# Optimization experiments

Hardware: AMD Instinct MI355X
Metric: run time of the kernel (lower is better)

The kernel has to match this reference:

```python
import jax, jax.numpy as jnp
import numpy as np

HEADS = 8
DIM_HEAD = 32
SCALE = DIM_HEAD ** -0.5


def setup_inputs() -> dict:
    key = jax.random.key(0)
    k1, k2, k3 = jax.random.split(key, 3)
    B, L, H, W, C = 2, 5, 100, 176, 256
    inner = HEADS * DIM_HEAD  # 256
    x = jax.random.normal(k1, (B, L, H, W, C), dtype=jnp.float32)
    mask = jnp.ones((B, H, W, 1, L), dtype=jnp.float32)
    W_qkv = jax.random.normal(k2, (C, 3 * inner), dtype=jnp.float32) * (C ** -0.5)
    W_out = jax.random.normal(k3, (inner, C), dtype=jnp.float32) * (inner ** -0.5)
    b_out = jnp.zeros((C,), dtype=jnp.float32)
    return {"x": x, "mask": mask, "W_qkv": W_qkv, "W_out": W_out, "b_out": b_out}


def _cav_attention(x, mask, W_qkv, W_out, b_out):
    B, L, H, W, C = x.shape
    # (B, L, H, W, C) -> (B, H, W, L, C)
    xp = jnp.transpose(x, (0, 2, 3, 1, 4))
    qkv = xp @ W_qkv  # (B,H,W,L,3*inner)
    q, k, v = jnp.split(qkv, 3, axis=-1)

    def to_heads(t):  # (B,H,W,L,m*c) -> (B,m,H,W,L,c)
        t = t.reshape(B, H, W, L, HEADS, DIM_HEAD)
        return jnp.transpose(t, (0, 4, 1, 2, 3, 5))

    q, k, v = to_heads(q), to_heads(k), to_heads(v)
    att = jnp.einsum('bmhwic,bmhwjc->bmhwij', q, k) * SCALE
    # mask: (B,H,W,1,L) -> broadcast over heads as (B,1,H,W,1,L)
    att = jnp.where(mask[:, None] == 0, -jnp.inf, att)
    att = jax.nn.softmax(att, axis=-1)
    out = jnp.einsum('bmhwij,bmhwjc->bmhwic', att, v)
    # (B,m,H,W,L,c) -> (B,H,W,L,m*c)
    out = jnp.transpose(out, (0, 2, 3, 4, 1, 5)).reshape(B, H, W, L, HEADS * DIM_HEAD)
    out = out @ W_out + b_out  # dropout is identity in eval mode
    # (B,H,W,L,C) -> (B,L,H,W,C)
    return jnp.transpose(out, (0, 3, 1, 2, 4))


def reference(x, mask, W_qkv, W_out, b_out):
    return _cav_attention(x, mask, W_qkv, W_out, b_out)
```

## Files before the change

kernel.cpp:

```cpp
#include <hip/hip_runtime.h>
#include <hip/hip_bf16.h>

#define LQ 5
#define HQ 100
#define WQ 176
#define HWQ 17600
#define TPB 16
#define ROWS 80
#define NBLK 2200
#define SCALE_QK 0.17677669529663687f

typedef __attribute__((ext_vector_type(8))) short bf16x8;
typedef __attribute__((ext_vector_type(4))) float f32x4;

__device__ __forceinline__ float bf2f(short s) {
  union { unsigned u; float f; } v;
  v.u = ((unsigned)(unsigned short)s) << 16;
  return v.f;
}
__device__ __forceinline__ unsigned short f2bf(float f) {
  union { float f; unsigned u; } v; v.f = f;
  unsigned r = (v.u + 0x7fffu + ((v.u >> 16) & 1u)) >> 16;
  return (unsigned short)r;
}

__global__ void prep_weights(const float* __restrict__ Wqkv,
                             const float* __restrict__ Wout,
                             unsigned short* __restrict__ WqkvT,
                             unsigned short* __restrict__ WoutT) {
  int idx = blockIdx.x * 256 + threadIdx.x;
  if (idx < 256 * 768) {
    int k = idx / 768, n = idx - k * 768;
    WqkvT[n * 256 + k] = f2bf(Wqkv[idx]);
  }
  if (idx < 256 * 256) {
    int k = idx >> 8, n = idx & 255;
    WoutT[n * 256 + k] = f2bf(Wout[idx]);
  }
}

#define SMEM_BYTES 149120

__global__ __launch_bounds__(256, 1)
void cav_attn_fused(const float* __restrict__ x,
                    const float* __restrict__ mask,
                    const unsigned short* __restrict__ WqkvT,
                    const unsigned short* __restrict__ WoutT,
                    const float* __restrict__ b_out,
                    float* __restrict__ out) {
  extern __shared__ char smem[];
  char* A_base = smem;
  char* O_base = smem + 40960;
  unsigned short* QKV = (unsigned short*)(smem + 81920);
  int*   gofs  = (int*)(smem + 148480);
  float* maskv = (float*)(smem + 148800);

  const int tid  = threadIdx.x;
  const int wave = tid >> 6;
  const int lane = tid & 63;
  const int lr   = lane & 15;
  const int lg   = lane >> 4;
  const int tile0 = blockIdx.x * TPB;

  if (tid < ROWS) {
    int tt = tid / LQ;
    int l  = tid - tt * LQ;
    int gt = tile0 + tt;
    int b  = gt / HWQ;
    int rem = gt - b * HWQ;
    int h  = rem / WQ;
    int w  = rem - h * WQ;
    gofs[tid]  = (((b * LQ + l) * HQ + h) * WQ + w) << 8;
    maskv[tid] = mask[((b * HQ + h) * WQ + w) * LQ + l];
  }
  __syncthreads();

  #pragma unroll
  for (int i = 0; i < 20; ++i) {
    int r  = i * 4 + wave;
    int kq = lane;
    f32x4 v = *(const f32x4*)(x + gofs[r] + kq * 4);
    ushort4 pk;
    pk.x = f2bf(v[0]); pk.y = f2bf(v[1]); pk.z = f2bf(v[2]); pk.w = f2bf(v[3]);
    int byte = r * 512 + kq * 8;
    byte ^= (r & 7) << 4;
    *(ushort4*)(A_base + byte) = pk;
  }
  __syncthreads();

  unsigned short* qbuf = QKV + wave * (ROWS * 104);

  #pragma unroll 1
  for (int hi = 0; hi < 2; ++hi) {
    const int head = wave * 2 + hi;
    f32x4 acc[6][5];
    #pragma unroll
    for (int j = 0; j < 6; ++j)
      #pragma unroll
      for (int mt = 0; mt < 5; ++mt)
        acc[j][mt] = (f32x4){0.f, 0.f, 0.f, 0.f};

    const int hb = head * 32;
    const int nb[6] = { hb, hb + 16, 256 + hb, 256 + hb + 16, 512 + hb, 512 + hb + 16 };

    #pragma unroll
    for (int kt = 0; kt < 8; ++kt) {
      bf16x8 a[5];
      #pragma unroll
      for (int mt = 0; mt < 5; ++mt) {
        int row = mt * 16 + lr;
        int byte = row * 512 + kt * 64 + lg * 16;
        byte ^= (row & 7) << 4;
        a[mt] = *(const bf16x8*)(A_base + byte);
      }
      #pragma unroll
      for (int j = 0; j < 6; ++j) {
        bf16x8 bfr = *(const bf16x8*)(WqkvT + (nb[j] + lr) * 256 + kt * 32 + lg * 8);
        #pragma unroll
        for (int mt = 0; mt < 5; ++mt)
          acc[j][mt] = __builtin_amdgcn_mfma_f32_16x16x32_bf16(a[mt], bfr, acc[j][mt], 0, 0, 0);
      }
    }

    __syncthreads();
    #pragma unroll
    for (int j = 0; j < 6; ++j)
      #pragma unroll
      for (int mt = 0; mt < 5; ++mt)
        #pragma unroll
        for (int rg = 0; rg < 4; ++rg) {
          int row = mt * 16 + lg * 4 + rg;
          qbuf[row * 104 + j * 16 + lr] = f2bf(acc[j][mt][rg]);
        }
    __syncthreads();

    #pragma unroll
    for (int ip = 0; ip < 2; ++ip) {
      const int t_ = (ip == 0) ? (lane >> 2) : lane;
      const int i_ = (ip == 0) ? (lane & 3) : 4;
      if (ip == 0 || lane < 16) {
        const int rq = t_ * 5 + i_;
        float q[32];
        #pragma unroll
        for (int ch = 0; ch < 4; ++ch) {
          bf16x8 qv = *(const bf16x8*)(qbuf + rq * 104 + ch * 8);
          #pragma unroll
          for (int e = 0; e < 8; ++e) q[ch * 8 + e] = bf2f(qv[e]);
        }
        float p[5];
        #pragma unroll
        for (int j = 0; j < 5; ++j) {
          const int rk = t_ * 5 + j;
          float d = 0.f;
          #pragma unroll
          for (int ch = 0; ch < 4; ++ch) {
            bf16x8 kv = *(const bf16x8*)(qbuf + rk * 104 + 32 + ch * 8);
            #pragma unroll
            for (int e = 0; e < 8; ++e) d += q[ch * 8 + e] * bf2f(kv[e]);
          }
          d *= SCALE_QK;
          p[j] = (maskv[rk] == 0.0f) ? -1e30f : d;
        }
        float mx = fmaxf(fmaxf(fmaxf(p[0], p[1]), fmaxf(p[2], p[3])), p[4]);
        float sum = 0.f;
        #pragma unroll
        for (int j = 0; j < 5; ++j) { p[j] = __expf(p[j] - mx); sum += p[j]; }
        const float inv = 1.0f / sum;
        float o[32];
        #pragma unroll
        for (int c = 0; c < 32; ++c) o[c] = 0.f;
        #pragma unroll
        for (int j = 0; j < 5; ++j) {
          const int rv = t_ * 5 + j;
          const float pj = p[j] * inv;
          #pragma unroll
          for (int ch = 0; ch < 4; ++ch) {
            bf16x8 vv = *(const bf16x8*)(qbuf + rv * 104 + 64 + ch * 8);
            #pragma unroll
            for (int e = 0; e < 8; ++e) o[ch * 8 + e] += pj * bf2f(vv[e]);
          }
        }
        #pragma unroll
        for (int ch = 0; ch < 8; ++ch) {
          ushort4 pk;
          pk.x = f2bf(o[ch * 4 + 0]); pk.y = f2bf(o[ch * 4 + 1]);
          pk.z = f2bf(o[ch * 4 + 2]); pk.w = f2bf(o[ch * 4 + 3]);
          int byte = rq * 512 + (head * 32 + ch * 4) * 2;
          byte ^= (rq & 7) << 4;
          *(ushort4*)(O_base + byte) = pk;
        }
      }
    }
  }
  __syncthreads();

  f32x4 acc2[4][5];
  #pragma unroll
  for (int j = 0; j < 4; ++j)
    #pragma unroll
    for (int mt = 0; mt < 5; ++mt)
      acc2[j][mt] = (f32x4){0.f, 0.f, 0.f, 0.f};

  #pragma unroll
  for (int kt = 0; kt < 8; ++kt) {
    bf16x8 a[5];
    #pragma unroll
    for (int mt = 0; mt < 5; ++mt) {
      int row = mt * 16 + lr;
      int byte = row * 512 + kt * 64 + lg * 16;
      byte ^= (row & 7) << 4;
      a[mt] = *(const bf16x8*)(O_base + byte);
    }
    #pragma unroll
    for (int j = 0; j < 4; ++j) {
      bf16x8 bfr = *(const bf16x8*)(WoutT + (wave * 64 + j * 16 + lr) * 256 + kt * 32 + lg * 8);
      #pragma unroll
      for (int mt = 0; mt < 5; ++mt)
        acc2[j][mt] = __builtin_amdgcn_mfma_f32_16x16x32_bf16(a[mt], bfr, acc2[j][mt], 0, 0, 0);
    }
  }

  #pragma unroll
  for (int j = 0; j < 4; ++j) {
    const int col = wave * 64 + j * 16 + lr;
    const float bo = b_out[col];
    #pragma unroll
    for (int mt = 0; mt < 5; ++mt)
      #pragma unroll
      for (int rg = 0; rg < 4; ++rg) {
        int row = mt * 16 + lg * 4 + rg;
        out[gofs[row] + col] = acc2[j][mt][rg] + bo;
      }
  }
}

extern "C" void kernel_launch(void* const* d_in, const int* in_sizes, int n_in,
                              void* d_out, int out_size, void* d_ws, size_t ws_size,
                              hipStream_t stream) {
  (void)in_sizes; (void)n_in; (void)out_size; (void)ws_size;
  const float* x     = (const float*)d_in[0];
  const float* mask  = (const float*)d_in[1];
  const float* Wqkv  = (const float*)d_in[2];
  const float* Wout  = (const float*)d_in[3];
  const float* bout  = (const float*)d_in[4];
  float* out = (float*)d_out;

  unsigned short* WqkvT = (unsigned short*)d_ws;
  unsigned short* WoutT = WqkvT + 768 * 256;

  (void)hipFuncSetAttribute((const void*)cav_attn_fused,
                            hipFuncAttributeMaxDynamicSharedMemorySize, SMEM_BYTES);

  prep_weights<<<768, 256, 0, stream>>>(Wqkv, Wout, WqkvT, WoutT);
  cav_attn_fused<<<NBLK, 256, SMEM_BYTES, stream>>>(x, mask, WqkvT, WoutT, bout, out);
}
```

Measured before the change: 386.5 us.

## Halve tokens per block for two blocks per CU and stage coalesced output stores

Each block now handles 8 tokens (40 rows) instead of 16, and shared memory is cut to about 74 KB so that two blocks fit per CU (launch bounds 2). The per-wave QKV staging no longer uses block-wide barriers, and attention runs in a single pass with one row per lane. The output tile goes through shared memory so global stores become row-contiguous f32x4 writes. In exchange, the MFMA tiles are padded from 40 to 48 rows, which adds wasted matrix work, and the padded rows read stale shared memory.

```diff
diff --git a/kernel.cpp b/kernel.cpp
--- a/kernel.cpp
+++ b/kernel.cpp
@@ -5,10 +5,18 @@
 #define HQ 100
 #define WQ 176
 #define HWQ 17600
-#define TPB 16
-#define ROWS 80
-#define NBLK 2200
+#define TPB 8
+#define ROWS 40
+#define NBLK 4400
 #define SCALE_QK 0.17677669529663687f
+
+#define A_OFF 0
+#define O_OFF 20480
+#define QKV_OFF 40960
+#define QBUF_STRIDE 8320
+#define GOFS_OFF 74240
+#define MASK_OFF 74400
+#define SMEM_BYTES 74560
 
 typedef __attribute__((ext_vector_type(8))) short bf16x8;
 typedef __attribute__((ext_vector_type(4))) float f32x4;
@@ -39,9 +47,7 @@
   }
 }
 
-#define SMEM_BYTES 149120
-
-__global__ __launch_bounds__(256, 1)
+__global__ __launch_bounds__(256, 2)
 void cav_attn_fused(const float* __restrict__ x,
                     const float* __restrict__ mask,
                     const unsigned short* __restrict__ WqkvT,
@@ -49,11 +55,10 @@
                     const float* __restrict__ b_out,
                     float* __restrict__ out) {
   extern __shared__ char smem[];
-  char* A_base = smem;
-  char* O_base = smem + 40960;
-  unsigned short* QKV = (unsigned short*)(smem + 81920);
-  int*   gofs  = (int*)(smem + 148480);
-  float* maskv = (float*)(smem + 148800);
+  char* A_base = smem + A_OFF;
+  char* O_base = smem + O_OFF;
+  int*   gofs  = (int*)(smem + GOFS_OFF);
+  float* maskv = (float*)(smem + MASK_OFF);
 
   const int tid  = threadIdx.x;
   const int wave = tid >> 6;
@@ -76,28 +81,27 @@
   __syncthreads();
 
   #pragma unroll
-  for (int i = 0; i < 20; ++i) {
+  for (int i = 0; i < 10; ++i) {
     int r  = i * 4 + wave;
-    int kq = lane;
-    f32x4 v = *(const f32x4*)(x + gofs[r] + kq * 4);
+    f32x4 v = *(const f32x4*)(x + gofs[r] + lane * 4);
     ushort4 pk;
     pk.x = f2bf(v[0]); pk.y = f2bf(v[1]); pk.z = f2bf(v[2]); pk.w = f2bf(v[3]);
-    int byte = r * 512 + kq * 8;
+    int byte = r * 512 + lane * 8;
     byte ^= (r & 7) << 4;
     *(ushort4*)(A_base + byte) = pk;
   }
   __syncthreads();
 
-  unsigned short* qbuf = QKV + wave * (ROWS * 104);
+  unsigned short* qbuf = (unsigned short*)(smem + QKV_OFF + wave * QBUF_STRIDE);
 
   #pragma unroll 1
   for (int hi = 0; hi < 2; ++hi) {
     const int head = wave * 2 + hi;
-    f32x4 acc[6][5];
+    f32x4 acc[6][3];
     #pragma unroll
     for (int j = 0; j < 6; ++j)
       #pragma unroll
-      for (int mt = 0; mt < 5; ++mt)
+      for (int mt = 0; mt < 3; ++mt)
         acc[j][mt] = (f32x4){0.f, 0.f, 0.f, 0.f};
 
     const int hb = head * 32;
@@ -105,9 +109,9 @@
 
     #pragma unroll
     for (int kt = 0; kt < 8; ++kt) {
-      bf16x8 a[5];
-      #pragma unroll
-      for (int mt = 0; mt < 5; ++mt) {
+      bf16x8 a[3];
+      #pragma unroll
+      for (int mt = 0; mt < 3; ++mt) {
         int row = mt * 16 + lr;
         int byte = row * 512 + kt * 64 + lg * 16;
         byte ^= (row & 7) << 4;
@@ -117,95 +121,90 @@
       for (int j = 0; j < 6; ++j) {
         bf16x8 bfr = *(const bf16x8*)(WqkvT + (nb[j] + lr) * 256 + kt * 32 + lg * 8);
         #pragma unroll
-        for (int mt = 0; mt < 5; ++mt)
+        for (int mt = 0; mt < 3; ++mt)
           acc[j][mt] = __builtin_amdgcn_mfma_f32_16x16x32_bf16(a[mt], bfr, acc[j][mt], 0, 0, 0);
       }
     }
 
-    __syncthreads();
     #pragma unroll
     for (int j = 0; j < 6; ++j)
       #pragma unroll
-      for (int mt = 0; mt < 5; ++mt)
+      for (int mt = 0; mt < 3; ++mt)
         #pragma unroll
         for (int rg = 0; rg < 4; ++rg) {
           int row = mt * 16 + lg * 4 + rg;
-          qbuf[row * 104 + j * 16 + lr] = f2bf(acc[j][mt][rg]);
+          if (row < ROWS)
+            qbuf[row * 104 + j * 16 + lr] = f2bf(acc[j][mt][rg]);
         }
-    __syncthreads();
-
-    #pragma unroll
-    for (int ip = 0; ip < 2; ++ip) {
-      const int t_ = (ip == 0) ? (lane >> 2) : lane;
-      const int i_ = (ip == 0) ? (lane & 3) : 4;
-      if (ip == 0 || lane < 16) {
-        const int rq = t_ * 5 + i_;
-        float q[32];
+
+    if (lane < ROWS) {
+      const int t_ = lane / 5;
+      const int rq = lane;
+      float q[32];
+      #pragma unroll
+      for (int ch = 0; ch < 4; ++ch) {
+        bf16x8 qv = *(const bf16x8*)(qbuf + rq * 104 + ch * 8);
+        #pragma unroll
+        for (int e = 0; e < 8; ++e) q[ch * 8 + e] = bf2f(qv[e]);
+      }
+      float p[5];
+      #pragma unroll
+      for (int j = 0; j < 5; ++j) {
+        const int rk = t_ * 5 + j;
+        float d = 0.f;
         #pragma unroll
         for (int ch = 0; ch < 4; ++ch) {
-          bf16x8 qv = *(const bf16x8*)(qbuf + rq * 104 + ch * 8);
+          bf16x8 kv = *(const bf16x8*)(qbuf + rk * 104 + 32 + ch * 8);
           #pragma unroll
-          for (int e = 0; e < 8; ++e) q[ch * 8 + e] = bf2f(qv[e]);
+          for (int e = 0; e < 8; ++e) d += q[ch * 8 + e] * bf2f(kv[e]);
         }
-        float p[5];
-        #pragma unroll
-        for (int j = 0; j < 5; ++j) {
-          const int rk = t_ * 5 + j;
-          float d = 0.f;
+        d *= SCALE_QK;
+        p[j] = (maskv[rk] == 0.0f) ? -1e30f : d;
+      }
+      float mx = fmaxf(fmaxf(fmaxf(p[0], p[1]), fmaxf(p[2], p[3])), p[4]);
+      float sum = 0.f;
+      #pragma unroll
+      for (int j = 0; j < 5; ++j) { p[j] = __expf(p[j] - mx); sum += p[j]; }
+      const float inv = 1.0f / sum;
+      float o[32];
+      #pragma unroll
+      for (int c = 0; c < 32; ++c) o[c] = 0.f;
+      #pragma unroll
+      for (int j = 0; j < 5; ++j) {
+        const int rv = t_ * 5 + j;
+        const float pj = p[j] * inv;
+        #pragma unroll
+        for (int ch = 0; ch < 4; ++ch) {
+          bf16x8 vv = *(const bf16x8*)(qbuf + rv * 104 + 64 + ch * 8);
           #pragma unroll
-          for (int ch = 0; ch < 4; ++ch) {
-            bf16x8 kv = *(const bf16x8*)(qbuf + rk * 104 + 32 + ch * 8);
-            #pragma unroll
-            for (int e = 0; e < 8; ++e) d += q[ch * 8 + e] * bf2f(kv[e]);
-          }
-          d *= SCALE_QK;
-          p[j] = (maskv[rk] == 0.0f) ? -1e30f : d;
+          for (int e = 0; e < 8; ++e) o[ch * 8 + e] += pj * bf2f(vv[e]);
         }
-        float mx = fmaxf(fmaxf(fmaxf(p[0], p[1]), fmaxf(p[2], p[3])), p[4]);
-        float sum = 0.f;
-        #pragma unroll
-        for (int j = 0; j < 5; ++j) { p[j] = __expf(p[j] - mx); sum += p[j]; }
-        const float inv = 1.0f / sum;
-        float o[32];
-        #pragma unroll
-        for (int c = 0; c < 32; ++c) o[c] = 0.f;
-        #pragma unroll
-        for (int j = 0; j < 5; ++j) {
-          const int rv = t_ * 5 + j;
-          const float pj = p[j] * inv;
-          #pragma unroll
-          for (int ch = 0; ch < 4; ++ch) {
-            bf16x8 vv = *(const bf16x8*)(qbuf + rv * 104 + 64 + ch * 8);
-            #pragma unroll
-            for (int e = 0; e < 8; ++e) o[ch * 8 + e] += pj * bf2f(vv[e]);
-          }
-        }
-        #pragma unroll
-        for (int ch = 0; ch < 8; ++ch) {
-          ushort4 pk;
-          pk.x = f2bf(o[ch * 4 + 0]); pk.y = f2bf(o[ch * 4 + 1]);
-          pk.z = f2bf(o[ch * 4 + 2]); pk.w = f2bf(o[ch * 4 + 3]);
-          int byte = rq * 512 + (head * 32 + ch * 4) * 2;
-          byte ^= (rq & 7) << 4;
-          *(ushort4*)(O_base + byte) = pk;
-        }
-      }
-    }
-  }
-  __syncthreads();
-
-  f32x4 acc2[4][5];
+      }
+      #pragma unroll
+      for (int ch = 0; ch < 8; ++ch) {
+        ushort4 pk;
+        pk.x = f2bf(o[ch * 4 + 0]); pk.y = f2bf(o[ch * 4 + 1]);
+        pk.z = f2bf(o[ch * 4 + 2]); pk.w = f2bf(o[ch * 4 + 3]);
+        int byte = rq * 512 + head * 64 + ch * 8;
+        byte ^= (rq & 7) << 4;
+        *(ushort4*)(O_base + byte) = pk;
+      }
+    }
+  }
+  __syncthreads();
+
+  f32x4 acc2[4][3];
   #pragma unroll
   for (int j = 0; j < 4; ++j)
     #pragma unroll
-    for (int mt = 0; mt < 5; ++mt)
+    for (int mt = 0; mt < 3; ++mt)
       acc2[j][mt] = (f32x4){0.f, 0.f, 0.f, 0.f};
 
   #pragma unroll
   for (int kt = 0; kt < 8; ++kt) {
-    bf16x8 a[5];
-    #pragma unroll
-    for (int mt = 0; mt < 5; ++mt) {
+    bf16x8 a[3];
+    #pragma unroll
+    for (int mt = 0; mt < 3; ++mt) {
       int row = mt * 16 + lr;
       int byte = row * 512 + kt * 64 + lg * 16;
       byte ^= (row & 7) << 4;
@@ -215,22 +214,31 @@
     for (int j = 0; j < 4; ++j) {
       bf16x8 bfr = *(const bf16x8*)(WoutT + (wave * 64 + j * 16 + lr) * 256 + kt * 32 + lg * 8);
       #pragma unroll
-      for (int mt = 0; mt < 5; ++mt)
+      for (int mt = 0; mt < 3; ++mt)
         acc2[j][mt] = __builtin_amdgcn_mfma_f32_16x16x32_bf16(a[mt], bfr, acc2[j][mt], 0, 0, 0);
     }
   }
+  __syncthreads();
 
   #pragma unroll
   for (int j = 0; j < 4; ++j) {
     const int col = wave * 64 + j * 16 + lr;
     const float bo = b_out[col];
     #pragma unroll
-    for (int mt = 0; mt < 5; ++mt)
+    for (int mt = 0; mt < 3; ++mt)
       #pragma unroll
       for (int rg = 0; rg < 4; ++rg) {
         int row = mt * 16 + lg * 4 + rg;
-        out[gofs[row] + col] = acc2[j][mt][rg] + bo;
-      }
+        if (row < ROWS)
+          *(float*)(smem + row * 1024 + col * 4) = acc2[j][mt][rg] + bo;
+      }
+  }
+  __syncthreads();
+  #pragma unroll
+  for (int i = 0; i < 10; ++i) {
+    int r = i * 4 + wave;
+    f32x4 v = *(const f32x4*)(smem + r * 1024 + lane * 16);
+    *(f32x4*)(out + gofs[r] + lane * 4) = v;
   }
 }
 
```

Result: faster. 345.2 us (-10.7%).
